# Performance work log

Measured on AMD Instinct MI355X. Metric: run time of the kernel, lower is better.

## Reference

```python
import jax, jax.numpy as jnp
import numpy as np

N = 100_000   # nodes
D = 128       # in_channels
H = 128       # hidden_channels
O = 128       # out_channels
M = 3_200_000 # adjacency nnz (avg degree 32)
E = 200_000   # query edges
P = 500_000   # common-neighbor pairs (padded, all valid here)
COS_EPS = 1e-8
DEG_EPS = 1e-6


def setup_inputs() -> dict:
    key = jax.random.key(0)
    ks = jax.random.split(key, 12)
    x = jax.random.normal(ks[0], (N, D), jnp.float32)
    adj_row = jnp.sort(jax.random.randint(ks[1], (M,), 0, N, jnp.int32))
    adj_col = jax.random.randint(ks[2], (M,), 0, N, jnp.int32)
    edges = jax.random.randint(ks[3], (2, E), 0, N, jnp.int32)
    cn_edge_idx = jnp.sort(jax.random.randint(ks[4], (P,), 0, E, jnp.int32))
    cn_node = jax.random.randint(ks[5], (P,), 0, N, jnp.int32)
    cn_valid = jnp.ones((P,), jnp.bool_)
    # MLP params (Kaiming-ish scale)
    W1 = jax.random.normal(ks[6], (D, H), jnp.float32) / np.sqrt(D)
    b1 = jnp.zeros((H,), jnp.float32)
    W2 = jax.random.normal(ks[7], (H, H), jnp.float32) / np.sqrt(H)
    b2 = jnp.zeros((H,), jnp.float32)
    W3 = jax.random.normal(ks[8], (H, O), jnp.float32) / np.sqrt(H)
    b3 = jnp.zeros((O,), jnp.float32)
    return dict(x=x, adj_row=adj_row, adj_col=adj_col, edges=edges,
                cn_edge_idx=cn_edge_idx, cn_node=cn_node, cn_valid=cn_valid,
                W1=W1, b1=b1, W2=W2, b2=b2, W3=W3, b3=b3)


def _cosine(a, b):
    # torch.nn.CosineSimilarity: dot / max(||a||*||b||, eps)
    dot = jnp.sum(a * b, axis=-1)
    na = jnp.sqrt(jnp.sum(a * a, axis=-1))
    nb = jnp.sqrt(jnp.sum(b * b, axis=-1))
    return dot / jnp.maximum(na * nb, COS_EPS)


def reference(x, adj_row, adj_col, edges, cn_edge_idx, cn_node, cn_valid,
              W1, b1, W2, b2, W3, b3):
    # degrees = adj.sum(-1) + 1e-6 (binary adjacency values)
    ones = jnp.ones(adj_row.shape[0], x.dtype)
    deg = jax.ops.segment_sum(ones, adj_row, num_segments=N) + DEG_EPS
    # x = x + (adj @ x) / deg[:, None]
    agg = jax.ops.segment_sum(x[adj_col], adj_row, num_segments=N)
    h = x + agg / deg[:, None]
    # MLP (BatchNorms are unused in the original forward; dropout = inference)
    h = jax.nn.relu(h @ W1 + b1)
    h = jax.nn.relu(h @ W2 + b2)
    h = h @ W3 + b3                      # [N, O]
    # gather per common-neighbor pair: u = edges[0][e], v = edges[1][e], c = neighbor
    u = edges[0][cn_edge_idx]
    v = edges[1][cn_edge_idx]
    hu, hv, hc = h[u], h[v], h[cn_node]  # [P, O] each
    w = _cosine(hu, hc) * _cosine(hv, hc)
    w = jnp.where(cn_valid, w, jnp.zeros((), h.dtype))
    # sparse row-sum over neighbors per query edge
    scores = jax.ops.segment_sum(w, cn_edge_idx, num_segments=E)
    return jax.nn.sigmoid(scores)
```

## Files before the change

### kernel.cpp

```cpp
#include <hip/hip_runtime.h>
#include <math.h>

constexpr int N_NODES = 100000;
constexpr int DIM     = 128;
constexpr int M_NNZ   = 3200000;
constexpr int E_EDGES = 200000;
constexpr int P_PAIRS = 500000;
constexpr int W_ELEMS = 3 * DIM * DIM;

typedef _Float16 half8  __attribute__((ext_vector_type(8)));
typedef _Float16 half4t __attribute__((ext_vector_type(4)));
typedef _Float16 half2t __attribute__((ext_vector_type(2)));
typedef float    f32x4  __attribute__((ext_vector_type(4)));
typedef float    f32x2  __attribute__((ext_vector_type(2)));
typedef unsigned int u32x2 __attribute__((ext_vector_type(2)));

#if defined(__has_builtin)
#  if __has_builtin(__builtin_amdgcn_cvt_scalef32_pk8_f16_fp8)
#    define HAVE_PK8 1
#  endif
#endif
#ifndef HAVE_PK8
#  define HAVE_PK8 0
#endif

__device__ inline half8 fp8x8_to_h8(u32x2 d) {
#if HAVE_PK8
    return __builtin_amdgcn_cvt_scalef32_pk8_f16_fp8(d, 1.0f);
#else
    f32x2 p0 = __builtin_amdgcn_cvt_pk_f32_fp8(d[0], false);
    f32x2 p1 = __builtin_amdgcn_cvt_pk_f32_fp8(d[0], true);
    f32x2 p2 = __builtin_amdgcn_cvt_pk_f32_fp8(d[1], false);
    f32x2 p3 = __builtin_amdgcn_cvt_pk_f32_fp8(d[1], true);
    return half8{(_Float16)p0[0], (_Float16)p0[1], (_Float16)p1[0], (_Float16)p1[1],
                 (_Float16)p2[0], (_Float16)p2[1], (_Float16)p3[0], (_Float16)p3[1]};
#endif
}

__device__ inline void stage_weight(const _Float16* __restrict__ src,
                                    _Float16* __restrict__ dst) {
    const int tid = threadIdx.x;
    #pragma unroll
    for (int j = 0; j < 8; ++j) {
        const int gg  = j * 256 + tid;
        const int row = gg >> 4, g = gg & 15;
        *(half8*)(dst + (row << 7) + ((g ^ (row & 15)) << 3)) =
            *(const half8*)(src + gg * 8);
    }
}

__device__ inline half8 ldsw(const _Float16* __restrict__ w,
                             int row, int q, int t, int l16) {
    return *(const half8*)(w + (row << 7) + (((q + 4 * t) ^ l16) << 3));
}

__global__ void prep_kernel(
    const float* __restrict__ W1, const float* __restrict__ W2,
    const float* __restrict__ W3, _Float16* __restrict__ Wt,
    const int* __restrict__ adj_row, int* __restrict__ rs, int* __restrict__ re,
    const int* __restrict__ cn_edge, int* __restrict__ es, int* __restrict__ ee) {
    const int tid = blockIdx.x * blockDim.x + threadIdx.x;
    if (tid < W_ELEMS) {
        int m = tid >> 14, n = (tid >> 7) & 127, k = tid & 127;
        const float* W = (m == 0) ? W1 : (m == 1) ? W2 : W3;
        Wt[tid] = (_Float16)W[k * DIM + n];
        return;
    }
    const int* arr; int len, nseg; int* s; int* e; int p;
    if (tid < W_ELEMS + M_NNZ) {
        arr = adj_row; len = M_NNZ; nseg = N_NODES; s = rs; e = re; p = tid - W_ELEMS;
    } else if (tid < W_ELEMS + M_NNZ + P_PAIRS) {
        arr = cn_edge; len = P_PAIRS; nseg = E_EDGES; s = es; e = ee; p = tid - W_ELEMS - M_NNZ;
    } else return;
    const int v = arr[p];
    if (p == 0) {
        s[v] = 0;
        for (int w = 0; w < v; ++w) { s[w] = 0; e[w] = 0; }
    } else {
        int pv = arr[p - 1];
        if (pv != v) {
            e[pv] = p; s[v] = p;
            for (int w = pv + 1; w < v; ++w) { s[w] = p; e[w] = p; }
        }
    }
    if (p == len - 1) {
        e[v] = len;
        for (int w = v + 1; w < nseg; ++w) { s[w] = len; e[w] = len; }
    }
}

__global__ __launch_bounds__(256) void gemm1_kernel(
    const float* __restrict__ x, const _Float16* __restrict__ Wt,
    _Float16* __restrict__ y, unsigned char* __restrict__ y8) {
    __shared__ __align__(16) _Float16 lw[16384];
    const int lane = threadIdx.x & 63;
    const int wave = threadIdx.x >> 6;
    const int q = lane >> 4, l16 = lane & 15;
    const int rBase = blockIdx.x * 128 + wave * 32;

    const int row0 = rBase + l16, row1 = rBase + 16 + l16;
    const int r0 = min(row0, N_NODES - 1), r1 = min(row1, N_NODES - 1);
    const float* Ap0 = x + (size_t)r0 * DIM + q * 8;
    const float* Ap1 = x + (size_t)r1 * DIM + q * 8;
    half8 a0[4], a1[4];
    #pragma unroll
    for (int t = 0; t < 4; ++t) {
        float4 u0 = *(const float4*)(Ap0 + t * 32);
        float4 u1 = *(const float4*)(Ap0 + t * 32 + 4);
        float4 w0 = *(const float4*)(Ap1 + t * 32);
        float4 w1 = *(const float4*)(Ap1 + t * 32 + 4);
        a0[t] = half8{(_Float16)u0.x, (_Float16)u0.y, (_Float16)u0.z, (_Float16)u0.w,
                      (_Float16)u1.x, (_Float16)u1.y, (_Float16)u1.z, (_Float16)u1.w};
        a1[t] = half8{(_Float16)w0.x, (_Float16)w0.y, (_Float16)w0.z, (_Float16)w0.w,
                      (_Float16)w1.x, (_Float16)w1.y, (_Float16)w1.z, (_Float16)w1.w};
    }
    stage_weight(Wt, lw);
    __syncthreads();

    #pragma unroll
    for (int c = 0; c < 8; ++c) {
        f32x4 acc0 = {0.f, 0.f, 0.f, 0.f}, acc1 = {0.f, 0.f, 0.f, 0.f};
        #pragma unroll
        for (int t = 0; t < 4; ++t) {
            const half8 w = ldsw(lw, c * 16 + l16, q, t, l16);
            acc0 = __builtin_amdgcn_mfma_f32_16x16x32_f16(w, a0[t], acc0, 0, 0, 0);
            acc1 = __builtin_amdgcn_mfma_f32_16x16x32_f16(w, a1[t], acc1, 0, 0, 0);
        }
        const int colBase = c * 16 + q * 4;
        half4t o0 = { (_Float16)acc0[0], (_Float16)acc0[1], (_Float16)acc0[2], (_Float16)acc0[3] };
        half4t o1 = { (_Float16)acc1[0], (_Float16)acc1[1], (_Float16)acc1[2], (_Float16)acc1[3] };
        int p0 = __builtin_amdgcn_cvt_pk_fp8_f32(acc0[0], acc0[1], 0, false);
        p0     = __builtin_amdgcn_cvt_pk_fp8_f32(acc0[2], acc0[3], p0, true);
        int p1 = __builtin_amdgcn_cvt_pk_fp8_f32(acc1[0], acc1[1], 0, false);
        p1     = __builtin_amdgcn_cvt_pk_fp8_f32(acc1[2], acc1[3], p1, true);
        if (row0 < N_NODES) {
            *(half4t*)(y + (size_t)row0 * DIM + colBase) = o0;
            *(int*)(y8 + (size_t)row0 * DIM + colBase) = p0;
        }
        if (row1 < N_NODES) {
            *(half4t*)(y + (size_t)row1 * DIM + colBase) = o1;
            *(int*)(y8 + (size_t)row1 * DIM + colBase) = p1;
        }
    }
}

__global__ __launch_bounds__(256) void agg_kernel(
    const _Float16* __restrict__ y, const unsigned char* __restrict__ y8,
    const int* __restrict__ rs, const int* __restrict__ re,
    const int* __restrict__ adj_col, const float* __restrict__ b1,
    _Float16* __restrict__ h1) {
    const int wave = threadIdx.x >> 6, lane = threadIdx.x & 63;
    const int node = blockIdx.x * 4 + wave;
    const int start = rs[node], cnt = re[node] - start;
    const int g = lane >> 4;
    const int l16 = lane & 15;
    const unsigned b8 = (unsigned)l16 * 8;

    float fa[8];
    half8 a0 = {}, a1 = {}, a2 = {}, a3 = {};
    for (int base = 0; base < cnt; base += 64) {
        const int chunk = min(64, cnt - base);
        const int colreg = adj_col[start + base + min(lane, chunk - 1)];
        int j = 0;
        for (; j + 16 <= chunk; j += 16) {
            int cc[4];
            #pragma unroll
            for (int s = 0; s < 4; ++s) cc[s] = __shfl(colreg, j + 4 * s + g);
            u32x2 dv[4];
            #pragma unroll
            for (int s = 0; s < 4; ++s)
                dv[s] = *(const u32x2*)(y8 + (((unsigned)cc[s] << 7) + b8));
            a0 += fp8x8_to_h8(dv[0]);
            a1 += fp8x8_to_h8(dv[1]);
            a2 += fp8x8_to_h8(dv[2]);
            a3 += fp8x8_to_h8(dv[3]);
        }
        for (; j < chunk; j += 4) {
            const int idx = j + g;
            const int c = __shfl(colreg, min(idx, chunk - 1));
            const u32x2 d = *(const u32x2*)(y8 + (((unsigned)c << 7) + b8));
            const half8 v = fp8x8_to_h8(d);
            if (idx < chunk) a0 += v;
        }
    }
    const half8 hs = (a0 + a1) + (a2 + a3);
    #pragma unroll
    for (int t = 0; t < 8; ++t) fa[t] = (float)hs[t];

    #pragma unroll
    for (int t = 0; t < 8; ++t) {
        float f = fa[t];
        f += __shfl_xor(f, 16);
        f += __shfl_xor(f, 32);
        fa[t] = f;
    }
    if (g == 0) {
        const float inv = 1.f / ((float)cnt + 1e-6f);
        const half8 sf = *(const half8*)(y + (size_t)node * DIM + b8);
        const float4 bb0 = *(const float4*)(b1 + b8);
        const float4 bb1 = *(const float4*)(b1 + b8 + 4);
        half8 o;
        #pragma unroll
        for (int t = 0; t < 8; ++t) {
            const float bb = (t < 4) ? ((const float*)&bb0)[t] : ((const float*)&bb1)[t - 4];
            o[t] = (_Float16)fmaxf((float)sf[t] + fa[t] * inv + bb, 0.f);
        }
        *(half8*)(h1 + (size_t)node * DIM + b8) = o;
    }
}

__global__ __launch_bounds__(256) void mlp23_kernel(
    const _Float16* __restrict__ h1, const _Float16* __restrict__ Wt,
    const float* __restrict__ b2, const float* __restrict__ b3,
    unsigned char* __restrict__ hN8) {
    __shared__ __align__(16) _Float16 lw[16384];
    __shared__ __align__(16) _Float16 tile[4][16][136];
    const int lane = threadIdx.x & 63;
    const int wave = threadIdx.x >> 6;
    const int q = lane >> 4, l16 = lane & 15;
    const int node = blockIdx.x * 64 + wave * 16 + l16;
    const int nl = min(node, N_NODES - 1);

    half8 aF[4];
    #pragma unroll
    for (int t = 0; t < 4; ++t)
        aF[t] = *(const half8*)(h1 + (size_t)nl * DIM + q * 8 + t * 32);

    stage_weight(Wt + 16384, lw);
    __syncthreads();

    half4t o2[8];
    #pragma unroll
    for (int c = 0; c < 8; ++c) {
        f32x4 acc = {0.f, 0.f, 0.f, 0.f};
        #pragma unroll
        for (int t = 0; t < 4; ++t) {
            const half8 w = ldsw(lw, c * 16 + l16, q, t, l16);
            acc = __builtin_amdgcn_mfma_f32_16x16x32_f16(w, aF[t], acc, 0, 0, 0);
        }
        const int colBase = c * 16 + q * 4;
        const float4 bb = *(const float4*)(b2 + colBase);
        o2[c] = half4t{ (_Float16)fmaxf(acc[0] + bb.x, 0.f),
                        (_Float16)fmaxf(acc[1] + bb.y, 0.f),
                        (_Float16)fmaxf(acc[2] + bb.z, 0.f),
                        (_Float16)fmaxf(acc[3] + bb.w, 0.f) };
    }
    __syncthreads();

    stage_weight(Wt + 32768, lw);

    #pragma unroll
    for (int c = 0; c < 8; ++c)
        *(half4t*)(&tile[wave][l16][c * 16 + q * 4]) = o2[c];
    #pragma unroll
    for (int t = 0; t < 4; ++t)
        aF[t] = *(const half8*)(&tile[wave][l16][q * 8 + t * 32]);

    __syncthreads();

    f32x4 vals[8];
    float s = 0.f;
    #pragma unroll
    for (int c = 0; c < 8; ++c) {
        f32x4 acc = {0.f, 0.f, 0.f, 0.f};
        #pragma unroll
        for (int t = 0; t < 4; ++t) {
            const half8 w = ldsw(lw, c * 16 + l16, q, t, l16);
            acc = __builtin_amdgcn_mfma_f32_16x16x32_f16(w, aF[t], acc, 0, 0, 0);
        }
        const int colBase = c * 16 + q * 4;
        const float4 bb = *(const float4*)(b3 + colBase);
        f32x4 v;
        v[0] = acc[0] + bb.x; v[1] = acc[1] + bb.y;
        v[2] = acc[2] + bb.z; v[3] = acc[3] + bb.w;
        s += v[0]*v[0] + v[1]*v[1] + v[2]*v[2] + v[3]*v[3];
        vals[c] = v;
    }
    s += __shfl_xor(s, 16);
    s += __shfl_xor(s, 32);
    const float rn = 1.f / fmaxf(sqrtf(s), 1e-4f);
    if (node < N_NODES) {
        #pragma unroll
        for (int c = 0; c < 8; ++c) {
            const int colBase = c * 16 + q * 4;
            int pk = __builtin_amdgcn_cvt_pk_fp8_f32(vals[c][0] * rn, vals[c][1] * rn, 0, false);
            pk     = __builtin_amdgcn_cvt_pk_fp8_f32(vals[c][2] * rn, vals[c][3] * rn, pk, true);
            *(int*)(hN8 + (((unsigned)node << 7) + colBase)) = pk;
        }
    }
}

__global__ __launch_bounds__(256) void edge_kernel(
    const unsigned char* __restrict__ h8,
    const int* __restrict__ edges, const int* __restrict__ es,
    const int* __restrict__ ee, const int* __restrict__ cn_node,
    float* __restrict__ out) {
    const int lane = threadIdx.x & 63;
    const int wave = threadIdx.x >> 6;
    const int g = lane >> 4, l16 = lane & 15;
    const int e = blockIdx.x * 16 + wave * 4 + g;
    const unsigned e8 = (unsigned)l16 * 8;

    const int start = es[e], end = ee[e];
    float sum = 0.f;
    if (end > start) {
        const int u = edges[e], v = edges[E_EDGES + e];
        const half8 hu = fp8x8_to_h8(*(const u32x2*)(h8 + (((unsigned)u << 7) + e8)));
        const half8 hv = fp8x8_to_h8(*(const u32x2*)(h8 + (((unsigned)v << 7) + e8)));
        half2t hu2[4], hv2[4];
        #pragma unroll
        for (int t = 0; t < 4; ++t) {
            hu2[t] = half2t{hu[2 * t], hu[2 * t + 1]};
            hv2[t] = half2t{hv[2 * t], hv[2 * t + 1]};
        }
        for (int p = start; p < end; p += 2) {
            const int i1 = p + 1;
            const int c0 = cn_node[p];
            const int c1 = cn_node[min(i1, end - 1)];
            const half8 hc0 = fp8x8_to_h8(*(const u32x2*)(h8 + (((unsigned)c0 << 7) + e8)));
            const half8 hc1 = fp8x8_to_h8(*(const u32x2*)(h8 + (((unsigned)c1 << 7) + e8)));
            float duc0 = 0.f, dvc0 = 0.f, duc1 = 0.f, dvc1 = 0.f;
            #pragma unroll
            for (int t = 0; t < 4; ++t) {
                half2t a = half2t{hc0[2 * t], hc0[2 * t + 1]};
                half2t b = half2t{hc1[2 * t], hc1[2 * t + 1]};
                duc0 = __builtin_amdgcn_fdot2(hu2[t], a, duc0, false);
                dvc0 = __builtin_amdgcn_fdot2(hv2[t], a, dvc0, false);
                duc1 = __builtin_amdgcn_fdot2(hu2[t], b, duc1, false);
                dvc1 = __builtin_amdgcn_fdot2(hv2[t], b, dvc1, false);
            }
            #pragma unroll
            for (int off = 1; off < 16; off <<= 1) {
                duc0 += __shfl_xor(duc0, off);
                dvc0 += __shfl_xor(dvc0, off);
                duc1 += __shfl_xor(duc1, off);
                dvc1 += __shfl_xor(dvc1, off);
            }
            sum += duc0 * dvc0;
            if (i1 < end) sum += duc1 * dvc1;
        }
    }
    if (l16 == 0) out[e] = 1.f / (1.f + expf(-sum));
}

extern "C" void kernel_launch(void* const* d_in, const int* in_sizes, int n_in,
                              void* d_out, int out_size, void* d_ws, size_t ws_size,
                              hipStream_t stream) {
    const float* x     = (const float*)d_in[0];
    const int* adj_row = (const int*)d_in[1];
    const int* adj_col = (const int*)d_in[2];
    const int* edges   = (const int*)d_in[3];
    const int* cn_edge = (const int*)d_in[4];
    const int* cn_node = (const int*)d_in[5];
    const float* W1 = (const float*)d_in[7];
    const float* b1 = (const float*)d_in[8];
    const float* W2 = (const float*)d_in[9];
    const float* b2 = (const float*)d_in[10];
    const float* W3 = (const float*)d_in[11];
    const float* b3 = (const float*)d_in[12];
    float* out = (float*)d_out;

    char* base = (char*)d_ws;
    _Float16* y  = (_Float16*)base;
    _Float16* h1 = (_Float16*)(base + 25600000);
    unsigned char* y8 = (unsigned char*)(base + 51200000);
    unsigned char* hN8 = y8;
    _Float16* Wt = (_Float16*)(base + 64000000);
    int* rs = (int*)(base + 64098304);
    int* re = (int*)(base + 64498304);
    int* es = (int*)(base + 64898304);
    int* ee = (int*)(base + 65698304);

    const int prep_threads = W_ELEMS + M_NNZ + P_PAIRS;
    prep_kernel<<<(prep_threads + 255) / 256, 256, 0, stream>>>(
        W1, W2, W3, Wt, adj_row, rs, re, cn_edge, es, ee);

    gemm1_kernel<<<(N_NODES + 127) / 128, 256, 0, stream>>>(x, Wt, y, y8);
    agg_kernel<<<N_NODES / 4, 256, 0, stream>>>(y, y8, rs, re, adj_col, b1, h1);
    mlp23_kernel<<<(N_NODES + 63) / 64, 256, 0, stream>>>(h1, Wt, b2, b3, hN8);
    edge_kernel<<<E_EDGES / 16, 256, 0, stream>>>(hN8, edges, es, ee, cn_node, out);
}
```

Baseline: 278.6 us.

## Parallelize edge scoring per pair with atomics and split aggregation launch

Replaces the per-edge loop over common-neighbor pairs with a per-pair kernel in which each 16-lane group scores one pair and atomically adds into the edge score, followed by a separate sigmoid pass. This removes the CSR segment-boundary construction for cn_edge from the prep kernel, which now zero-fills the output instead. The aggregation kernel is also split into two half-range launches. The cost is redundant loads of the u/v rows for every pair, float atomics with non-deterministic summation order, and two extra kernel launches.

```diff
diff --git a/kernel.cpp b/kernel.cpp
--- a/kernel.cpp
+++ b/kernel.cpp
@@ -58,7 +58,7 @@
     const float* __restrict__ W1, const float* __restrict__ W2,
     const float* __restrict__ W3, _Float16* __restrict__ Wt,
     const int* __restrict__ adj_row, int* __restrict__ rs, int* __restrict__ re,
-    const int* __restrict__ cn_edge, int* __restrict__ es, int* __restrict__ ee) {
+    float* __restrict__ out) {
     const int tid = blockIdx.x * blockDim.x + threadIdx.x;
     if (tid < W_ELEMS) {
         int m = tid >> 14, n = (tid >> 7) & 127, k = tid & 127;
@@ -66,26 +66,27 @@
         Wt[tid] = (_Float16)W[k * DIM + n];
         return;
     }
-    const int* arr; int len, nseg; int* s; int* e; int p;
     if (tid < W_ELEMS + M_NNZ) {
-        arr = adj_row; len = M_NNZ; nseg = N_NODES; s = rs; e = re; p = tid - W_ELEMS;
-    } else if (tid < W_ELEMS + M_NNZ + P_PAIRS) {
-        arr = cn_edge; len = P_PAIRS; nseg = E_EDGES; s = es; e = ee; p = tid - W_ELEMS - M_NNZ;
-    } else return;
-    const int v = arr[p];
-    if (p == 0) {
-        s[v] = 0;
-        for (int w = 0; w < v; ++w) { s[w] = 0; e[w] = 0; }
-    } else {
-        int pv = arr[p - 1];
-        if (pv != v) {
-            e[pv] = p; s[v] = p;
-            for (int w = pv + 1; w < v; ++w) { s[w] = p; e[w] = p; }
-        }
-    }
-    if (p == len - 1) {
-        e[v] = len;
-        for (int w = v + 1; w < nseg; ++w) { s[w] = len; e[w] = len; }
+        const int p = tid - W_ELEMS;
+        const int v = adj_row[p];
+        if (p == 0) {
+            rs[v] = 0;
+            for (int w = 0; w < v; ++w) { rs[w] = 0; re[w] = 0; }
+        } else {
+            int pv = adj_row[p - 1];
+            if (pv != v) {
+                re[pv] = p; rs[v] = p;
+                for (int w = pv + 1; w < v; ++w) { rs[w] = p; re[w] = p; }
+            }
+        }
+        if (p == M_NNZ - 1) {
+            re[v] = M_NNZ;
+            for (int w = v + 1; w < N_NODES; ++w) { rs[w] = M_NNZ; re[w] = M_NNZ; }
+        }
+        return;
+    }
+    if (tid < W_ELEMS + M_NNZ + E_EDGES) {
+        out[tid - W_ELEMS - M_NNZ] = 0.f;
     }
 }
 
@@ -148,9 +149,9 @@
     const _Float16* __restrict__ y, const unsigned char* __restrict__ y8,
     const int* __restrict__ rs, const int* __restrict__ re,
     const int* __restrict__ adj_col, const float* __restrict__ b1,
-    _Float16* __restrict__ h1) {
+    _Float16* __restrict__ h1, int node_base) {
     const int wave = threadIdx.x >> 6, lane = threadIdx.x & 63;
-    const int node = blockIdx.x * 4 + wave;
+    const int node = node_base + blockIdx.x * 4 + wave;
     const int start = rs[node], cnt = re[node] - start;
     const int g = lane >> 4;
     const int l16 = lane & 15;
@@ -290,57 +291,40 @@
     }
 }
 
-__global__ __launch_bounds__(256) void edge_kernel(
+__global__ __launch_bounds__(256) void edge_pair_kernel(
     const unsigned char* __restrict__ h8,
-    const int* __restrict__ edges, const int* __restrict__ es,
-    const int* __restrict__ ee, const int* __restrict__ cn_node,
-    float* __restrict__ out) {
+    const int* __restrict__ edges, const int* __restrict__ cn_edge,
+    const int* __restrict__ cn_node, float* __restrict__ scores) {
     const int lane = threadIdx.x & 63;
     const int wave = threadIdx.x >> 6;
     const int g = lane >> 4, l16 = lane & 15;
-    const int e = blockIdx.x * 16 + wave * 4 + g;
+    const int p = blockIdx.x * 16 + wave * 4 + g;
     const unsigned e8 = (unsigned)l16 * 8;
 
-    const int start = es[e], end = ee[e];
-    float sum = 0.f;
-    if (end > start) {
-        const int u = edges[e], v = edges[E_EDGES + e];
-        const half8 hu = fp8x8_to_h8(*(const u32x2*)(h8 + (((unsigned)u << 7) + e8)));
-        const half8 hv = fp8x8_to_h8(*(const u32x2*)(h8 + (((unsigned)v << 7) + e8)));
-        half2t hu2[4], hv2[4];
-        #pragma unroll
-        for (int t = 0; t < 4; ++t) {
-            hu2[t] = half2t{hu[2 * t], hu[2 * t + 1]};
-            hv2[t] = half2t{hv[2 * t], hv[2 * t + 1]};
-        }
-        for (int p = start; p < end; p += 2) {
-            const int i1 = p + 1;
-            const int c0 = cn_node[p];
-            const int c1 = cn_node[min(i1, end - 1)];
-            const half8 hc0 = fp8x8_to_h8(*(const u32x2*)(h8 + (((unsigned)c0 << 7) + e8)));
-            const half8 hc1 = fp8x8_to_h8(*(const u32x2*)(h8 + (((unsigned)c1 << 7) + e8)));
-            float duc0 = 0.f, dvc0 = 0.f, duc1 = 0.f, dvc1 = 0.f;
-            #pragma unroll
-            for (int t = 0; t < 4; ++t) {
-                half2t a = half2t{hc0[2 * t], hc0[2 * t + 1]};
-                half2t b = half2t{hc1[2 * t], hc1[2 * t + 1]};
-                duc0 = __builtin_amdgcn_fdot2(hu2[t], a, duc0, false);
-                dvc0 = __builtin_amdgcn_fdot2(hv2[t], a, dvc0, false);
-                duc1 = __builtin_amdgcn_fdot2(hu2[t], b, duc1, false);
-                dvc1 = __builtin_amdgcn_fdot2(hv2[t], b, dvc1, false);
-            }
-            #pragma unroll
-            for (int off = 1; off < 16; off <<= 1) {
-                duc0 += __shfl_xor(duc0, off);
-                dvc0 += __shfl_xor(dvc0, off);
-                duc1 += __shfl_xor(duc1, off);
-                dvc1 += __shfl_xor(dvc1, off);
-            }
-            sum += duc0 * dvc0;
-            if (i1 < end) sum += duc1 * dvc1;
-        }
-    }
-    if (l16 == 0) out[e] = 1.f / (1.f + expf(-sum));
+    const int e = cn_edge[p];
+    const int c = cn_node[p];
+    const int u = edges[e], v = edges[E_EDGES + e];
+    const half8 hc = fp8x8_to_h8(*(const u32x2*)(h8 + (((unsigned)c << 7) + e8)));
+    const half8 hu = fp8x8_to_h8(*(const u32x2*)(h8 + (((unsigned)u << 7) + e8)));
+    const half8 hv = fp8x8_to_h8(*(const u32x2*)(h8 + (((unsigned)v << 7) + e8)));
+    float du = 0.f, dv = 0.f;
+    #pragma unroll
+    for (int t = 0; t < 4; ++t) {
+        const half2t a = half2t{hc[2 * t], hc[2 * t + 1]};
+        du = __builtin_amdgcn_fdot2(half2t{hu[2 * t], hu[2 * t + 1]}, a, du, false);
+        dv = __builtin_amdgcn_fdot2(half2t{hv[2 * t], hv[2 * t + 1]}, a, dv, false);
+    }
+    #pragma unroll
+    for (int off = 1; off < 16; off <<= 1) {
+        du += __shfl_xor(du, off);
+        dv += __shfl_xor(dv, off);
+    }
+    if (l16 == 0) atomicAdd(scores + e, du * dv);
+}
+
+__global__ void sigmoid_kernel(float* __restrict__ out) {
+    const int e = blockIdx.x * blockDim.x + threadIdx.x;
+    if (e < E_EDGES) out[e] = 1.f / (1.f + expf(-out[e]));
 }
 
 extern "C" void kernel_launch(void* const* d_in, const int* in_sizes, int n_in,
@@ -368,15 +352,15 @@
     _Float16* Wt = (_Float16*)(base + 64000000);
     int* rs = (int*)(base + 64098304);
     int* re = (int*)(base + 64498304);
-    int* es = (int*)(base + 64898304);
-    int* ee = (int*)(base + 65698304);
-
-    const int prep_threads = W_ELEMS + M_NNZ + P_PAIRS;
+
+    const int prep_threads = W_ELEMS + M_NNZ + E_EDGES;
     prep_kernel<<<(prep_threads + 255) / 256, 256, 0, stream>>>(
-        W1, W2, W3, Wt, adj_row, rs, re, cn_edge, es, ee);
+        W1, W2, W3, Wt, adj_row, rs, re, out);
 
     gemm1_kernel<<<(N_NODES + 127) / 128, 256, 0, stream>>>(x, Wt, y, y8);
-    agg_kernel<<<N_NODES / 4, 256, 0, stream>>>(y, y8, rs, re, adj_col, b1, h1);
+    agg_kernel<<<N_NODES / 8, 256, 0, stream>>>(y, y8, rs, re, adj_col, b1, h1, 0);
+    agg_kernel<<<N_NODES / 8, 256, 0, stream>>>(y, y8, rs, re, adj_col, b1, h1, N_NODES / 2);
     mlp23_kernel<<<(N_NODES + 63) / 64, 256, 0, stream>>>(h1, Wt, b2, b3, hN8);
-    edge_kernel<<<E_EDGES / 16, 256, 0, stream>>>(hN8, edges, es, ee, cn_node, out);
-}
+    edge_pair_kernel<<<P_PAIRS / 16, 256, 0, stream>>>(hN8, edges, cn_edge, cn_node, out);
+    sigmoid_kernel<<<(E_EDGES + 255) / 256, 256, 0, stream>>>(out);
+}
```

New measurement: 287.2 us. 3.1% more time.
